# Kernel tuning notes

Hardware: AMD Instinct MI355X
Metric: run time of the kernel (lower is better)

## Reference

```python
import jax, jax.numpy as jnp
import numpy as np

N_NODES = 100000


def setup_inputs() -> dict:
    key = jax.random.key(0)
    k1, k2, k3 = jax.random.split(key, 3)
    x = jax.random.normal(k1, (N_NODES, 64), dtype=jnp.float32)
    edge_index = jax.random.randint(k2, (2, 1600000), 0, N_NODES, dtype=jnp.int64)
    W = jax.random.normal(k3, (64, 64), dtype=jnp.float32) * (1.0 / np.sqrt(64.0))
    b = jnp.zeros((64,), dtype=jnp.float32)
    prelu_a = jnp.full((1,), 0.25, dtype=jnp.float32)
    return {"x": x, "edge_index": edge_index, "W": W, "b": b, "prelu_a": prelu_a}


def reference(x, edge_index, W, b, prelu_a):
    N = x.shape[0]
    # GCNConv default: add self-loops with weight 1, symmetric normalization.
    loop = jnp.arange(N, dtype=edge_index.dtype)
    src = jnp.concatenate([edge_index[0], loop])  # [E+N]
    dst = jnp.concatenate([edge_index[1], loop])  # [E+N]
    ew = jnp.ones(src.shape[0], dtype=x.dtype)
    deg = jax.ops.segment_sum(ew, dst, num_segments=N)  # in-degree at targets
    dinv = jnp.where(deg > 0, jax.lax.rsqrt(deg), 0.0)
    norm = dinv[src] * dinv[dst]  # [E+N]
    xw = x @ W  # linear transform first (as in GCNConv)
    msg = xw[src] * norm[:, None]  # gather + scale, [E+N, out]
    out = jax.ops.segment_sum(msg, dst, num_segments=N) + b
    # PReLU with single shared slope
    return jnp.where(out >= 0, out, prelu_a[0] * out)
```

## Files before the change

### kernel.cpp

```cpp
#include <hip/hip_runtime.h>
#include <hip/hip_fp16.h>


static inline int iceil(long long a, int b) { return (int)((a + (long long)b - 1) / b); }

#define CAP 4096
#define NBUK_MAX 1024
#define SCTH 1024
#define BUFK 8

__global__ void k_detect(const int* __restrict__ ei, long long n_i32_min,
                         int* __restrict__ flag, int* __restrict__ gcur, int nbuk) {
    __shared__ int nz;
    if (threadIdx.x == 0) nz = 0;
    __syncthreads();
    long long half = n_i32_min >> 1;
    long long step = half / 1024;
    if (step == 0) step = 1;
    for (int t = threadIdx.x; t < 1024; t += blockDim.x) {
        long long k = (long long)t * step;
        if (k < half && ei[2 * k + 1] != 0) nz = 1;
    }
    for (int b = threadIdx.x; b < nbuk; b += blockDim.x) gcur[b] = b * CAP;
    __syncthreads();
    if (threadIdx.x == 0) *flag = nz ? 1 : 2;
}

__global__ __launch_bounds__(SCTH) void k_scat(const int* __restrict__ ei,
                                               const int* __restrict__ flag,
                                               int* __restrict__ gcur,
                                               int* __restrict__ part,
                                               long long E, int nbuk, int chunk) {
    __shared__ int hist[NBUK_MAX];
    __shared__ int sbase[NBUK_MAX];
    const int t = threadIdx.x;
    for (int i = t; i < nbuk; i += SCTH) hist[i] = 0;
    __syncthreads();
    const int st = *flag;
    const long long beg = (long long)blockIdx.x * chunk;
    long long end = beg + chunk; if (end > E) end = E;

    int bs[BUFK], bd[BUFK];
#pragma unroll
    for (int kk = 0; kk < BUFK; ++kk) {
        long long e = beg + t + (long long)kk * SCTH;
        bool v = e < end;
        bs[kk] = v ? ei[e * st] : 0;
        bd[kk] = v ? ei[(E + e) * st] : -1;
    }
#pragma unroll
    for (int kk = 0; kk < BUFK; ++kk)
        if (bd[kk] >= 0) atomicAdd(&hist[bd[kk] >> 7], 1);
    __syncthreads();
    for (int i = t; i < nbuk; i += SCTH) {
        int c = hist[i];
        sbase[i] = c ? atomicAdd(&gcur[i], c) : 0;
        hist[i] = 0;
    }
    __syncthreads();
#pragma unroll
    for (int kk = 0; kk < BUFK; ++kk) {
        if (bd[kk] >= 0) {
            int b = bd[kk] >> 7;
            int r = atomicAdd(&hist[b], 1);
            part[sbase[b] + r] = ((bd[kk] & 127) << 17) | bs[kk];
        }
    }
}

__global__ __launch_bounds__(256) void k_gemmmeta(const int* __restrict__ part,
                                                  const int* __restrict__ gcur,
                                                  const float* __restrict__ x,
                                                  const float* __restrict__ W,
                                                  int2* __restrict__ meta,
                                                  __half* __restrict__ xwsh, int N) {
    __shared__ float Ws[64 * 64];
    __shared__ float xT[64][132];
    __shared__ int cnt[128], inc[128];
    __shared__ float dinvL[128];
    const int tid = threadIdx.x;
    const int bb = blockIdx.x;
    const int tile0 = bb * 128;

    if (tid < 128) cnt[tid] = 0;
    __syncthreads();

    {
        const float4* W4 = (const float4*)W;
        float4* Ws4 = (float4*)Ws;
#pragma unroll
        for (int j = 0; j < 4; ++j) Ws4[tid + 256 * j] = W4[tid + 256 * j];
        const int lr = tid >> 4;
        const int c4 = (tid & 15) * 4;
#pragma unroll
        for (int i = 0; i < 8; ++i) {
            int row = lr + 16 * i;
            int gr = tile0 + row;
            if (gr >= N) gr = N - 1;
            float4 v = *(const float4*)(x + (long long)gr * 64 + c4);
            xT[c4 + 0][row] = v.x;
            xT[c4 + 1][row] = v.y;
            xT[c4 + 2][row] = v.z;
            xT[c4 + 3][row] = v.w;
        }
    }
    {
        const int beg = bb * CAP, end = gcur[bb];
        for (int i = beg + tid; i < end; i += 256)
            atomicAdd(&cnt[(part[i] >> 17) & 127], 1);
    }
    __syncthreads();
    if (tid < 128) inc[tid] = cnt[tid];
    __syncthreads();
    for (int off = 1; off < 128; off <<= 1) {
        int v = (tid < 128 && tid >= off) ? inc[tid - off] : 0;
        __syncthreads();
        if (tid < 128) inc[tid] += v;
        __syncthreads();
    }
    if (tid < 128) {
        dinvL[tid] = rsqrtf((float)cnt[tid] + 1.0f);
        int d = tile0 + tid;
        if (d < N) meta[d] = make_int2(cnt[tid], inc[tid] - cnt[tid]);
    }
    __syncthreads();

    const int ri = tid >> 4;
    const int ci = tid & 15;
    float acc[8][4];
#pragma unroll
    for (int j = 0; j < 8; ++j)
#pragma unroll
        for (int c = 0; c < 4; ++c) acc[j][c] = 0.0f;
#pragma unroll 4
    for (int k = 0; k < 64; ++k) {
        float4 xa = *(const float4*)&xT[k][8 * ri];
        float4 xb = *(const float4*)&xT[k][8 * ri + 4];
        float4 wv = *(const float4*)&Ws[k * 64 + 4 * ci];
        float xr[8] = {xa.x, xa.y, xa.z, xa.w, xb.x, xb.y, xb.z, xb.w};
        float wc[4] = {wv.x, wv.y, wv.z, wv.w};
#pragma unroll
        for (int j = 0; j < 8; ++j)
#pragma unroll
            for (int c = 0; c < 4; ++c) acc[j][c] = fmaf(xr[j], wc[c], acc[j][c]);
    }
#pragma unroll
    for (int j = 0; j < 8; ++j) {
        int gr = tile0 + 8 * ri + j;
        if (gr < N) {
            float di = dinvL[8 * ri + j];
            __half2 h01 = __floats2half2_rn(acc[j][0] * di, acc[j][1] * di);
            __half2 h23 = __floats2half2_rn(acc[j][2] * di, acc[j][3] * di);
            uint2 u;
            u.x = *(unsigned int*)&h01;
            u.y = *(unsigned int*)&h23;
            *(uint2*)(xwsh + (long long)gr * 64 + 4 * ci) = u;
        }
    }
}

__global__ __launch_bounds__(512) void k_gfuse(const int* __restrict__ part,
                                               const int* __restrict__ gcur,
                                               const int2* __restrict__ meta,
                                               const __half* __restrict__ xwsh,
                                               const float* __restrict__ b,
                                               const float* __restrict__ pa,
                                               float* __restrict__ out, int N) {
    __shared__ int cnt[128], exc[128], rnk[128];
    __shared__ int lcsr[CAP];
    const int t = threadIdx.x;
    const int bb = blockIdx.x;
    const int beg = bb * CAP, end = gcur[bb];
    const int tile0 = bb * 128;
    if (t < 128) {
        int d = tile0 + t;
        int2 m = (d < N) ? meta[d] : make_int2(0, 0);
        cnt[t] = m.x;
        exc[t] = m.y;
        rnk[t] = 0;
    }
    __syncthreads();
    for (int i = beg + t; i < end; i += 512) {
        int v = part[i];
        int dl = (v >> 17) & 127;
        int r = atomicAdd(&rnk[dl], 1);
        lcsr[exc[dl] + r] = v & 0x1FFFF;
    }
    __syncthreads();

    const int lane = t & 63;
    const int g = lane >> 4;
    const int fl = lane & 15;
    const int wib = t >> 6;
    const int q = wib * 4 + g;
    const float slope = pa[0];
    const float4 b4 = ((const float4*)b)[fl];

    for (int dl = q; dl < 128; dl += 32) {
        int d = tile0 + dl;
        if (d >= N) break;
        const int jb = exc[dl];
        const int n = cnt[dl];
        float ax = 0.f, ay = 0.f, az = 0.f, aw = 0.f;
        int j = 0;
        for (; j + 7 < n; j += 8) {
            int s0 = lcsr[jb + j],     s1 = lcsr[jb + j + 1];
            int s2 = lcsr[jb + j + 2], s3 = lcsr[jb + j + 3];
            int s4 = lcsr[jb + j + 4], s5 = lcsr[jb + j + 5];
            int s6 = lcsr[jb + j + 6], s7 = lcsr[jb + j + 7];
            uint2 u0 = *(const uint2*)(xwsh + (long long)s0 * 64 + 4 * fl);
            uint2 u1 = *(const uint2*)(xwsh + (long long)s1 * 64 + 4 * fl);
            uint2 u2 = *(const uint2*)(xwsh + (long long)s2 * 64 + 4 * fl);
            uint2 u3 = *(const uint2*)(xwsh + (long long)s3 * 64 + 4 * fl);
            uint2 u4 = *(const uint2*)(xwsh + (long long)s4 * 64 + 4 * fl);
            uint2 u5 = *(const uint2*)(xwsh + (long long)s5 * 64 + 4 * fl);
            uint2 u6 = *(const uint2*)(xwsh + (long long)s6 * 64 + 4 * fl);
            uint2 u7 = *(const uint2*)(xwsh + (long long)s7 * 64 + 4 * fl);
            float2 f0a = __half22float2(*(const __half2*)&u0.x);
            float2 f0b = __half22float2(*(const __half2*)&u0.y);
            float2 f1a = __half22float2(*(const __half2*)&u1.x);
            float2 f1b = __half22float2(*(const __half2*)&u1.y);
            float2 f2a = __half22float2(*(const __half2*)&u2.x);
            float2 f2b = __half22float2(*(const __half2*)&u2.y);
            float2 f3a = __half22float2(*(const __half2*)&u3.x);
            float2 f3b = __half22float2(*(const __half2*)&u3.y);
            float2 f4a = __half22float2(*(const __half2*)&u4.x);
            float2 f4b = __half22float2(*(const __half2*)&u4.y);
            float2 f5a = __half22float2(*(const __half2*)&u5.x);
            float2 f5b = __half22float2(*(const __half2*)&u5.y);
            float2 f6a = __half22float2(*(const __half2*)&u6.x);
            float2 f6b = __half22float2(*(const __half2*)&u6.y);
            float2 f7a = __half22float2(*(const __half2*)&u7.x);
            float2 f7b = __half22float2(*(const __half2*)&u7.y);
            ax += ((f0a.x + f1a.x) + (f2a.x + f3a.x)) +
                  ((f4a.x + f5a.x) + (f6a.x + f7a.x));
            ay += ((f0a.y + f1a.y) + (f2a.y + f3a.y)) +
                  ((f4a.y + f5a.y) + (f6a.y + f7a.y));
            az += ((f0b.x + f1b.x) + (f2b.x + f3b.x)) +
                  ((f4b.x + f5b.x) + (f6b.x + f7b.x));
            aw += ((f0b.y + f1b.y) + (f2b.y + f3b.y)) +
                  ((f4b.y + f5b.y) + (f6b.y + f7b.y));
        }
        for (; j + 3 < n; j += 4) {
            int s0 = lcsr[jb + j],     s1 = lcsr[jb + j + 1];
            int s2 = lcsr[jb + j + 2], s3 = lcsr[jb + j + 3];
            uint2 u0 = *(const uint2*)(xwsh + (long long)s0 * 64 + 4 * fl);
            uint2 u1 = *(const uint2*)(xwsh + (long long)s1 * 64 + 4 * fl);
            uint2 u2 = *(const uint2*)(xwsh + (long long)s2 * 64 + 4 * fl);
            uint2 u3 = *(const uint2*)(xwsh + (long long)s3 * 64 + 4 * fl);
            float2 f0a = __half22float2(*(const __half2*)&u0.x);
            float2 f0b = __half22float2(*(const __half2*)&u0.y);
            float2 f1a = __half22float2(*(const __half2*)&u1.x);
            float2 f1b = __half22float2(*(const __half2*)&u1.y);
            float2 f2a = __half22float2(*(const __half2*)&u2.x);
            float2 f2b = __half22float2(*(const __half2*)&u2.y);
            float2 f3a = __half22float2(*(const __half2*)&u3.x);
            float2 f3b = __half22float2(*(const __half2*)&u3.y);
            ax += (f0a.x + f1a.x) + (f2a.x + f3a.x);
            ay += (f0a.y + f1a.y) + (f2a.y + f3a.y);
            az += (f0b.x + f1b.x) + (f2b.x + f3b.x);
            aw += (f0b.y + f1b.y) + (f2b.y + f3b.y);
        }
        for (; j < n; ++j) {
            int s = lcsr[jb + j];
            uint2 u = *(const uint2*)(xwsh + (long long)s * 64 + 4 * fl);
            float2 f01 = __half22float2(*(const __half2*)&u.x);
            float2 f23 = __half22float2(*(const __half2*)&u.y);
            ax += f01.x; ay += f01.y; az += f23.x; aw += f23.y;
        }
        uint2 u = *(const uint2*)(xwsh + (long long)d * 64 + 4 * fl);
        float2 s01 = __half22float2(*(const __half2*)&u.x);
        float2 s23 = __half22float2(*(const __half2*)&u.y);
        float di = rsqrtf((float)n + 1.0f);
        float4 v;
        v.x = di * (ax + s01.x) + b4.x;
        v.y = di * (ay + s01.y) + b4.y;
        v.z = di * (az + s23.x) + b4.z;
        v.w = di * (aw + s23.y) + b4.w;
        v.x = v.x >= 0.f ? v.x : slope * v.x;
        v.y = v.y >= 0.f ? v.y : slope * v.y;
        v.z = v.z >= 0.f ? v.z : slope * v.z;
        v.w = v.w >= 0.f ? v.w : slope * v.w;
        *(float4*)(out + (long long)d * 64 + 4 * fl) = v;
    }
}

extern "C" void kernel_launch(void* const* d_in, const int* in_sizes, int n_in,
                              void* d_out, int out_size, void* d_ws, size_t ws_size,
                              hipStream_t stream) {
    const float* x  = (const float*)d_in[0];
    const int*   ei = (const int*)d_in[1];
    const float* W  = (const float*)d_in[2];
    const float* b  = (const float*)d_in[3];
    const float* pa = (const float*)d_in[4];
    float* out = (float*)d_out;

    const int N = in_sizes[0] / 64;
    const long long E = (long long)in_sizes[1] / 2;
    const int nbuk = (N + 127) >> 7;
    int nscat = iceil(E, SCTH * BUFK);
    if (nscat < 256) nscat = 256;
    const int chunk = iceil(E, nscat);

    char* ws = (char*)d_ws;
    size_t o = 0;
    int*    flag  = (int*)(ws + o);   o += 256;
    int*    gcur  = (int*)(ws + o);   o += ((size_t)nbuk * 4 + 255) & ~(size_t)255;
    int2*   meta  = (int2*)(ws + o);  o += ((size_t)N * 8 + 255) & ~(size_t)255;
    int*    part  = (int*)(ws + o);   o += ((size_t)nbuk * CAP * 4 + 255) & ~(size_t)255;
    __half* xwsh  = (__half*)(ws + o);

    k_detect<<<1, 256, 0, stream>>>(ei, (long long)in_sizes[1], flag, gcur, nbuk);
    k_scat<<<nscat, SCTH, 0, stream>>>(ei, flag, gcur, part, E, nbuk, chunk);
    k_gemmmeta<<<nbuk, 256, 0, stream>>>(part, gcur, x, W, meta, xwsh, N);
    k_gfuse<<<nbuk, 512, 0, stream>>>(part, gcur, meta, xwsh, b, pa, out, N);
}
```

Measured before the change: 86.73 us.

## Use MFMA fp16 for the feature transform and fold dtype detection into scatter

```diff
diff --git a/kernel.cpp b/kernel.cpp
--- a/kernel.cpp
+++ b/kernel.cpp
@@ -9,34 +9,26 @@
 #define SCTH 1024
 #define BUFK 8
 
-__global__ void k_detect(const int* __restrict__ ei, long long n_i32_min,
-                         int* __restrict__ flag, int* __restrict__ gcur, int nbuk) {
-    __shared__ int nz;
-    if (threadIdx.x == 0) nz = 0;
-    __syncthreads();
-    long long half = n_i32_min >> 1;
-    long long step = half / 1024;
-    if (step == 0) step = 1;
-    for (int t = threadIdx.x; t < 1024; t += blockDim.x) {
-        long long k = (long long)t * step;
-        if (k < half && ei[2 * k + 1] != 0) nz = 1;
-    }
-    for (int b = threadIdx.x; b < nbuk; b += blockDim.x) gcur[b] = b * CAP;
-    __syncthreads();
-    if (threadIdx.x == 0) *flag = nz ? 1 : 2;
-}
+typedef __attribute__((ext_vector_type(8))) _Float16 half8;
+typedef __attribute__((ext_vector_type(4))) float floatx4;
 
 __global__ __launch_bounds__(SCTH) void k_scat(const int* __restrict__ ei,
-                                               const int* __restrict__ flag,
                                                int* __restrict__ gcur,
                                                int* __restrict__ part,
-                                               long long E, int nbuk, int chunk) {
+                                               long long E, int nbuk, int chunk,
+                                               long long n_i32) {
     __shared__ int hist[NBUK_MAX];
     __shared__ int sbase[NBUK_MAX];
     const int t = threadIdx.x;
+    long long half = n_i32 >> 1;
+    long long step = half >> 6;
+    if (step == 0) step = 1;
+    long long sk = (long long)(t & 63) * step;
+    int sample = (sk < half) ? ei[2 * sk + 1] : 0;
+    const int st = __any(sample != 0) ? 1 : 2;
+
     for (int i = t; i < nbuk; i += SCTH) hist[i] = 0;
     __syncthreads();
-    const int st = *flag;
     const long long beg = (long long)blockIdx.x * chunk;
     long long end = beg + chunk; if (end > E) end = E;
 
@@ -54,7 +46,7 @@
     __syncthreads();
     for (int i = t; i < nbuk; i += SCTH) {
         int c = hist[i];
-        sbase[i] = c ? atomicAdd(&gcur[i], c) : 0;
+        sbase[i] = c ? (i * CAP + atomicAdd(&gcur[i], c)) : 0;
         hist[i] = 0;
     }
     __syncthreads();
@@ -74,8 +66,7 @@
                                                   const float* __restrict__ W,
                                                   int2* __restrict__ meta,
                                                   __half* __restrict__ xwsh, int N) {
-    __shared__ float Ws[64 * 64];
-    __shared__ float xT[64][132];
+    __shared__ _Float16 Wth[64 * 64];
     __shared__ int cnt[128], inc[128];
     __shared__ float dinvL[128];
     const int tid = threadIdx.x;
@@ -87,25 +78,20 @@
 
     {
         const float4* W4 = (const float4*)W;
-        float4* Ws4 = (float4*)Ws;
-#pragma unroll
-        for (int j = 0; j < 4; ++j) Ws4[tid + 256 * j] = W4[tid + 256 * j];
-        const int lr = tid >> 4;
-        const int c4 = (tid & 15) * 4;
-#pragma unroll
-        for (int i = 0; i < 8; ++i) {
-            int row = lr + 16 * i;
-            int gr = tile0 + row;
-            if (gr >= N) gr = N - 1;
-            float4 v = *(const float4*)(x + (long long)gr * 64 + c4);
-            xT[c4 + 0][row] = v.x;
-            xT[c4 + 1][row] = v.y;
-            xT[c4 + 2][row] = v.z;
-            xT[c4 + 3][row] = v.w;
+#pragma unroll
+        for (int j = 0; j < 4; ++j) {
+            int idx = tid + 256 * j;
+            float4 v = W4[idx];
+            int k = idx >> 4;
+            int n0 = (idx & 15) * 4;
+            Wth[(n0 + 0) * 64 + k] = (_Float16)v.x;
+            Wth[(n0 + 1) * 64 + k] = (_Float16)v.y;
+            Wth[(n0 + 2) * 64 + k] = (_Float16)v.z;
+            Wth[(n0 + 3) * 64 + k] = (_Float16)v.w;
         }
     }
     {
-        const int beg = bb * CAP, end = gcur[bb];
+        const int beg = bb * CAP, end = bb * CAP + gcur[bb];
         for (int i = beg + tid; i < end; i += 256)
             atomicAdd(&cnt[(part[i] >> 17) & 127], 1);
     }
@@ -125,36 +111,50 @@
     }
     __syncthreads();
 
-    const int ri = tid >> 4;
-    const int ci = tid & 15;
-    float acc[8][4];
-#pragma unroll
-    for (int j = 0; j < 8; ++j)
-#pragma unroll
-        for (int c = 0; c < 4; ++c) acc[j][c] = 0.0f;
-#pragma unroll 4
-    for (int k = 0; k < 64; ++k) {
-        float4 xa = *(const float4*)&xT[k][8 * ri];
-        float4 xb = *(const float4*)&xT[k][8 * ri + 4];
-        float4 wv = *(const float4*)&Ws[k * 64 + 4 * ci];
-        float xr[8] = {xa.x, xa.y, xa.z, xa.w, xb.x, xb.y, xb.z, xb.w};
-        float wc[4] = {wv.x, wv.y, wv.z, wv.w};
-#pragma unroll
-        for (int j = 0; j < 8; ++j)
-#pragma unroll
-            for (int c = 0; c < 4; ++c) acc[j][c] = fmaf(xr[j], wc[c], acc[j][c]);
-    }
-#pragma unroll
-    for (int j = 0; j < 8; ++j) {
-        int gr = tile0 + 8 * ri + j;
-        if (gr < N) {
-            float di = dinvL[8 * ri + j];
-            __half2 h01 = __floats2half2_rn(acc[j][0] * di, acc[j][1] * di);
-            __half2 h23 = __floats2half2_rn(acc[j][2] * di, acc[j][3] * di);
-            uint2 u;
-            u.x = *(unsigned int*)&h01;
-            u.y = *(unsigned int*)&h23;
-            *(uint2*)(xwsh + (long long)gr * 64 + 4 * ci) = u;
+    const int lane = tid & 63;
+    const int w = tid >> 6;
+    const int mrow = lane & 15;
+    const int kq = lane >> 4;
+
+    half8 bf[4][2];
+#pragma unroll
+    for (int ct = 0; ct < 4; ++ct)
+#pragma unroll
+        for (int ks = 0; ks < 2; ++ks)
+            bf[ct][ks] = *(const half8*)&Wth[(ct * 16 + mrow) * 64 + ks * 32 + kq * 8];
+
+#pragma unroll
+    for (int p = 0; p < 2; ++p) {
+        const int rt = w * 2 + p;
+        int gr = tile0 + rt * 16 + mrow;
+        if (gr >= N) gr = N - 1;
+        const float* xr = x + (long long)gr * 64 + kq * 8;
+        float4 u0 = *(const float4*)xr;
+        float4 u1 = *(const float4*)(xr + 4);
+        float4 u2 = *(const float4*)(xr + 32);
+        float4 u3 = *(const float4*)(xr + 36);
+        half8 a0, a1;
+        a0[0] = (_Float16)u0.x; a0[1] = (_Float16)u0.y;
+        a0[2] = (_Float16)u0.z; a0[3] = (_Float16)u0.w;
+        a0[4] = (_Float16)u1.x; a0[5] = (_Float16)u1.y;
+        a0[6] = (_Float16)u1.z; a0[7] = (_Float16)u1.w;
+        a1[0] = (_Float16)u2.x; a1[1] = (_Float16)u2.y;
+        a1[2] = (_Float16)u2.z; a1[3] = (_Float16)u2.w;
+        a1[4] = (_Float16)u3.x; a1[5] = (_Float16)u3.y;
+        a1[6] = (_Float16)u3.z; a1[7] = (_Float16)u3.w;
+#pragma unroll
+        for (int ct = 0; ct < 4; ++ct) {
+            floatx4 acc = {0.f, 0.f, 0.f, 0.f};
+            acc = __builtin_amdgcn_mfma_f32_16x16x32_f16(a0, bf[ct][0], acc, 0, 0, 0);
+            acc = __builtin_amdgcn_mfma_f32_16x16x32_f16(a1, bf[ct][1], acc, 0, 0, 0);
+#pragma unroll
+            for (int r = 0; r < 4; ++r) {
+                int m = rt * 16 + kq * 4 + r;
+                int d = tile0 + m;
+                if (d < N)
+                    xwsh[(long long)d * 64 + ct * 16 + mrow] =
+                        __float2half(acc[r] * dinvL[m]);
+            }
         }
     }
 }
@@ -170,7 +170,7 @@
     __shared__ int lcsr[CAP];
     const int t = threadIdx.x;
     const int bb = blockIdx.x;
-    const int beg = bb * CAP, end = gcur[bb];
+    const int beg = bb * CAP, end = bb * CAP + gcur[bb];
     const int tile0 = bb * 128;
     if (t < 128) {
         int d = tile0 + t;
@@ -304,14 +304,14 @@
 
     char* ws = (char*)d_ws;
     size_t o = 0;
-    int*    flag  = (int*)(ws + o);   o += 256;
     int*    gcur  = (int*)(ws + o);   o += ((size_t)nbuk * 4 + 255) & ~(size_t)255;
     int2*   meta  = (int2*)(ws + o);  o += ((size_t)N * 8 + 255) & ~(size_t)255;
     int*    part  = (int*)(ws + o);   o += ((size_t)nbuk * CAP * 4 + 255) & ~(size_t)255;
     __half* xwsh  = (__half*)(ws + o);
 
-    k_detect<<<1, 256, 0, stream>>>(ei, (long long)in_sizes[1], flag, gcur, nbuk);
-    k_scat<<<nscat, SCTH, 0, stream>>>(ei, flag, gcur, part, E, nbuk, chunk);
+    hipMemsetAsync(gcur, 0, (size_t)nbuk * 4, stream);
+    k_scat<<<nscat, SCTH, 0, stream>>>(ei, gcur, part, E, nbuk, chunk,
+                                       (long long)in_sizes[1]);
     k_gemmmeta<<<nbuk, 256, 0, stream>>>(part, gcur, x, W, meta, xwsh, N);
     k_gfuse<<<nbuk, 512, 0, stream>>>(part, gcur, meta, xwsh, b, pa, out, N);
 }
```

New measurement: 80.20 us. -7.5%, faster.
